# Performance work log

Measured on AMD Instinct MI355X. Metric: run time of the kernel, lower is better.

## Reference

```python
import jax, jax.numpy as jnp
import numpy as np


def setup_inputs() -> dict:
    key = jax.random.key(0)
    k1, k2, k3, k4 = jax.random.split(key, 4)
    B, T, C, H = 8, 2048, 768, 64
    x = jax.random.normal(k1, (B, T, C), dtype=jnp.float32)
    # nn.Linear(n_embd, head_size, bias=False): weight [H, C]; stored here as [C, H] for x @ W
    Wk = jax.random.normal(k2, (C, H), dtype=jnp.float32) * (C ** -0.5)
    Wq = jax.random.normal(k3, (C, H), dtype=jnp.float32) * (C ** -0.5)
    Wv = jax.random.normal(k4, (C, H), dtype=jnp.float32) * (C ** -0.5)
    return {"x": x, "Wk": Wk, "Wq": Wq, "Wv": Wv}


def reference(x, Wk, Wq, Wv):
    # x: [B, T, C]
    C = x.shape[-1]
    k = jnp.einsum("btc,ch->bth", x, Wk)  # [B, T, H]
    q = jnp.einsum("btc,ch->bth", x, Wq)  # [B, T, H]
    v = jnp.einsum("btc,ch->bth", x, Wv)  # [B, T, H]
    # NOTE: source scales by C**-0.5 where C = n_embd (input channels), not head_size
    wei = jnp.einsum("bth,bsh->bts", q, k) * (C ** -0.5)  # [B, T, T]
    wei = jax.nn.softmax(wei, axis=-1)
    # dropout p=0.0 (eval): identity
    out = jnp.einsum("bts,bsh->bth", wei, v)  # [B, T, H]
    return out
```

## Files before the change

kernel.cpp:

```cpp
#include <hip/hip_runtime.h>


typedef __attribute__((ext_vector_type(4))) float f32x4;
typedef __attribute__((ext_vector_type(8))) unsigned short u16x8;
typedef __attribute__((ext_vector_type(8))) __bf16 bf16x8;
typedef __attribute__((ext_vector_type(8))) _Float16 f16x8;

#define LDR 72
#define LDT 40
#define KSCALE (0.03608439182435161f * 1.4426950408889634f)
#define PBIAS 4.0f

__device__ __forceinline__ unsigned short f2bf(float f) {
  unsigned int u = __float_as_uint(f);
  u += 0x7FFFu + ((u >> 16) & 1u);
  return (unsigned short)(u >> 16);
}
__device__ __forceinline__ unsigned short hi16(float f) {
  return (unsigned short)(__float_as_uint(f) >> 16);
}
__device__ __forceinline__ f32x4 mfma_bf16(u16x8 a, u16x8 b, f32x4 c) {
  return __builtin_amdgcn_mfma_f32_16x16x32_bf16(
      __builtin_bit_cast(bf16x8, a), __builtin_bit_cast(bf16x8, b), c, 0, 0, 0);
}
__device__ __forceinline__ void cp32B(unsigned short* dst, const unsigned short* src) {
  *(u16x8*)dst = *(const u16x8*)src;
  *(u16x8*)(dst + 8) = *(const u16x8*)(src + 8);
}

__global__ __launch_bounds__(256) void wconv_k(const float* __restrict__ Wk,
                                               const float* __restrict__ Wq,
                                               const float* __restrict__ Wv,
                                               unsigned short* __restrict__ wt) {
  __shared__ unsigned short tr[64 * LDR];
  const int w = blockIdx.x / 12;
  const int kt = blockIdx.x - w * 12;
  const float* W = (w == 0) ? Wk : ((w == 1) ? Wq : Wv);
  const int tid = threadIdx.x;
  const int kr = tid >> 2;
  const int n0 = (tid & 3) * 16;
  const f32x4* src = (const f32x4*)(W + (size_t)(kt * 64 + kr) * 64 + n0);
  f32x4 a0 = src[0], a1 = src[1], a2 = src[2], a3 = src[3];
#pragma unroll
  for (int j = 0; j < 4; ++j) {
    tr[(n0 + j) * LDR + kr] = f2bf(a0[j]);
    tr[(n0 + 4 + j) * LDR + kr] = f2bf(a1[j]);
    tr[(n0 + 8 + j) * LDR + kr] = f2bf(a2[j]);
    tr[(n0 + 12 + j) * LDR + kr] = f2bf(a3[j]);
  }
  __syncthreads();
  const int n = tid >> 2, kc = (tid & 3) * 16;
  cp32B(&wt[(size_t)(w * 64 + n) * 768 + kt * 64 + kc], &tr[n * LDR + kc]);
}

__global__ __launch_bounds__(256) void proj_k(const float* __restrict__ x,
                                              const unsigned short* __restrict__ wt,
                                              unsigned short* __restrict__ kg,
                                              unsigned short* __restrict__ qg,
                                              unsigned short* __restrict__ vt) {
  __shared__ unsigned short x_s[32 * LDR];
  __shared__ unsigned short w_s[192 * LDR];
  __shared__ unsigned short vt_s[64 * LDT];
  const int tid = threadIdx.x;
  const int wv = tid >> 6, lane = tid & 63, c = lane & 15, quad = lane >> 4;
  const int m0 = blockIdx.x * 32;
  const int rowg = wv & 1;
  const int nfb = (wv >> 1) * 6;
  const int srow = tid >> 3;
  const int sc8 = (tid & 7) * 8;

  f32x4 acc[6];
#pragma unroll
  for (int i = 0; i < 6; ++i) acc[i] = f32x4{0.f, 0.f, 0.f, 0.f};

  f32x4 xf0, xf1;
  u16x8 wf[6];
  {
    const f32x4* s = (const f32x4*)(x + (size_t)(m0 + srow) * 768 + sc8);
    xf0 = s[0]; xf1 = s[1];
  }
#pragma unroll
  for (int i = 0; i < 6; ++i)
    wf[i] = *(const u16x8*)&wt[(size_t)(srow + 32 * i) * 768 + sc8];

  for (int kc = 0; kc < 768; kc += 64) {
    {
      u16x8 u;
#pragma unroll
      for (int j = 0; j < 4; ++j) { u[j] = f2bf(xf0[j]); u[4 + j] = f2bf(xf1[j]); }
      *(u16x8*)&x_s[srow * LDR + sc8] = u;
    }
#pragma unroll
    for (int i = 0; i < 6; ++i)
      *(u16x8*)&w_s[(srow + 32 * i) * LDR + sc8] = wf[i];
    __syncthreads();
    if (kc + 64 < 768) {
      const f32x4* s = (const f32x4*)(x + (size_t)(m0 + srow) * 768 + kc + 64 + sc8);
      xf0 = s[0]; xf1 = s[1];
#pragma unroll
      for (int i = 0; i < 6; ++i)
        wf[i] = *(const u16x8*)&wt[(size_t)(srow + 32 * i) * 768 + kc + 64 + sc8];
    }
#pragma unroll
    for (int k32 = 0; k32 < 2; ++k32) {
      u16x8 a = *(const u16x8*)&x_s[(rowg * 16 + c) * LDR + k32 * 32 + quad * 8];
#pragma unroll
      for (int j = 0; j < 6; ++j) {
        u16x8 b = *(const u16x8*)&w_s[((nfb + j) * 16 + c) * LDR + k32 * 32 + quad * 8];
        acc[j] = mfma_bf16(a, b, acc[j]);
      }
    }
    __syncthreads();
  }
  const int r0 = rowg * 16 + quad * 4;
#pragma unroll
  for (int j = 0; j < 6; ++j) {
    const int nf = nfb + j;
    if (nf < 4) {
#pragma unroll
      for (int r = 0; r < 4; ++r)
        kg[(size_t)(m0 + r0 + r) * 64 + nf * 16 + c] = f2bf(acc[j][r]);
    } else if (nf < 8) {
#pragma unroll
      for (int r = 0; r < 4; ++r)
        qg[(size_t)(m0 + r0 + r) * 64 + (nf - 4) * 16 + c] = f2bf(acc[j][r] * KSCALE);
    } else {
#pragma unroll
      for (int r = 0; r < 4; ++r)
        vt_s[((nf - 8) * 16 + c) * LDT + r0 + r] = f2bf(acc[j][r]);
    }
  }
  __syncthreads();
  {
    const int h = tid >> 2, c8 = (tid & 3) * 8;
    const int b = m0 >> 11, tb = m0 & 2047;
    *(u16x8*)(vt + (size_t)b * 131072 + (size_t)h * 2048 + tb + c8) =
        *(const u16x8*)&vt_s[h * LDT + c8];
  }
}

__global__ __launch_bounds__(256, 4) void attn_k(const unsigned short* __restrict__ qg,
                                                 const unsigned short* __restrict__ kg,
                                                 const unsigned short* __restrict__ vt,
                                                 _Float16* __restrict__ part,
                                                 float* __restrict__ lsum) {
  __shared__ unsigned short k_s[64 * LDR];
  __shared__ unsigned short v_s[64 * LDR];
  __shared__ unsigned short p_s[64 * LDR];
  const int tid = threadIdx.x;
  const int wv = tid >> 6, lane = tid & 63, c = lane & 15, quad = lane >> 4;
  const int bq = blockIdx.x;
  const int qt = blockIdx.y;
  const int sc = blockIdx.z;
  const int tq0 = qt * 64;
  const int srow = tid >> 2, sch = (tid & 3) * 16;
  const int s_beg = sc << 9, s_end = s_beg + 512;

  const unsigned short* kbase = kg + (size_t)bq * 131072;
  const unsigned short* vbase = vt + (size_t)bq * 131072;

  u16x8 aq[2];
#pragma unroll
  for (int k32 = 0; k32 < 2; ++k32)
    aq[k32] = *(const u16x8*)(qg + (size_t)(bq * 2048 + tq0 + wv * 16 + c) * 64 +
                              k32 * 32 + quad * 8);

  u16x8 kb0 = *(const u16x8*)(kbase + (size_t)(s_beg + srow) * 64 + sch);
  u16x8 kb1 = *(const u16x8*)(kbase + (size_t)(s_beg + srow) * 64 + sch + 8);
  u16x8 vb0 = *(const u16x8*)(vbase + (size_t)srow * 2048 + s_beg + sch);
  u16x8 vb1 = *(const u16x8*)(vbase + (size_t)srow * 2048 + s_beg + sch + 8);

  u16x8 ones;
#pragma unroll
  for (int j = 0; j < 8; ++j) ones[j] = 0x3F80;

  f32x4 o_acc[4], l_acc;
#pragma unroll
  for (int hf = 0; hf < 4; ++hf) o_acc[hf] = f32x4{0.f, 0.f, 0.f, 0.f};
  l_acc = f32x4{0.f, 0.f, 0.f, 0.f};

  for (int s0 = s_beg; s0 < s_end; s0 += 64) {
    *(u16x8*)&k_s[srow * LDR + sch] = kb0;
    *(u16x8*)&k_s[srow * LDR + sch + 8] = kb1;
    *(u16x8*)&v_s[srow * LDR + sch] = vb0;
    *(u16x8*)&v_s[srow * LDR + sch + 8] = vb1;
    __syncthreads();
    if (s0 + 64 < s_end) {
      kb0 = *(const u16x8*)(kbase + (size_t)(s0 + 64 + srow) * 64 + sch);
      kb1 = *(const u16x8*)(kbase + (size_t)(s0 + 64 + srow) * 64 + sch + 8);
      vb0 = *(const u16x8*)(vbase + (size_t)srow * 2048 + s0 + 64 + sch);
      vb1 = *(const u16x8*)(vbase + (size_t)srow * 2048 + s0 + 64 + sch + 8);
    }
    f32x4 sacc[4];
#pragma unroll
    for (int nf = 0; nf < 4; ++nf) sacc[nf] = f32x4{0.f, 0.f, 0.f, 0.f};
#pragma unroll
    for (int k32 = 0; k32 < 2; ++k32) {
#pragma unroll
      for (int nf = 0; nf < 4; ++nf) {
        u16x8 b = *(const u16x8*)&k_s[(nf * 16 + c) * LDR + k32 * 32 + quad * 8];
        sacc[nf] = mfma_bf16(aq[k32], b, sacc[nf]);
      }
    }
    const int prow = wv * 16 + quad * 4;
#pragma unroll
    for (int nf = 0; nf < 4; ++nf)
#pragma unroll
      for (int r = 0; r < 4; ++r)
        p_s[(prow + r) * LDR + ((nf ^ quad) * 16) + c] =
            hi16(__builtin_amdgcn_exp2f(sacc[nf][r] - PBIAS));
    asm volatile("s_waitcnt lgkmcnt(0)" ::: "memory");
#pragma unroll
    for (int k32 = 0; k32 < 2; ++k32) {
      const int chunkP = (2 * k32 + (quad >> 1)) ^ (c >> 2);
      u16x8 ap = *(const u16x8*)&p_s[(wv * 16 + c) * LDR + chunkP * 16 + (quad & 1) * 8];
#pragma unroll
      for (int hf = 0; hf < 4; ++hf) {
        u16x8 bv = *(const u16x8*)&v_s[(hf * 16 + c) * LDR + k32 * 32 + quad * 8];
        o_acc[hf] = mfma_bf16(ap, bv, o_acc[hf]);
      }
      l_acc = mfma_bf16(ap, ones, l_acc);
    }
    __syncthreads();
  }
  const int pbase = (bq * 32 + qt) * 4 + sc;
  _Float16* po = part + (size_t)pbase * 4096;
#pragma unroll
  for (int hf = 0; hf < 4; ++hf)
#pragma unroll
    for (int r = 0; r < 4; ++r)
      po[(wv * 16 + quad * 4 + r) * 64 + hf * 16 + c] = (_Float16)o_acc[hf][r];
  if (c == 0) {
#pragma unroll
    for (int r = 0; r < 4; ++r)
      lsum[pbase * 64 + wv * 16 + quad * 4 + r] = l_acc[r];
  }
}

__global__ __launch_bounds__(256) void comb_k(const _Float16* __restrict__ part,
                                              const float* __restrict__ lsum,
                                              float* __restrict__ out) {
  const int bq = blockIdx.x, qh = blockIdx.y;
  const int qt = qh >> 1;
  const int row = (qh & 1) * 32 + (threadIdx.x >> 3);
  const int h0 = (threadIdx.x & 7) * 8;
  const int base = (bq * 32 + qt) * 4;
  float acc[8];
#pragma unroll
  for (int j = 0; j < 8; ++j) acc[j] = 0.f;
  float l = 0.f;
#pragma unroll
  for (int c4 = 0; c4 < 4; ++c4) {
    l += lsum[(base + c4) * 64 + row];
    f16x8 p = *(const f16x8*)(part + (size_t)(base + c4) * 4096 + row * 64 + h0);
#pragma unroll
    for (int j = 0; j < 8; ++j) acc[j] += (float)p[j];
  }
  const float inv = 1.0f / l;
  float* op = out + (size_t)(bq * 2048 + qt * 64 + row) * 64 + h0;
#pragma unroll
  for (int j = 0; j < 8; ++j) op[j] = acc[j] * inv;
}

extern "C" void kernel_launch(void* const* d_in, const int* in_sizes, int n_in,
                              void* d_out, int out_size, void* d_ws, size_t ws_size,
                              hipStream_t stream) {
  const float* x = (const float*)d_in[0];
  const float* Wk = (const float*)d_in[1];
  const float* Wq = (const float*)d_in[2];
  const float* Wv = (const float*)d_in[3];
  char* ws = (char*)d_ws;
  unsigned short* kg = (unsigned short*)(ws);
  unsigned short* qg = (unsigned short*)(ws + (size_t)(2 << 20));
  unsigned short* vt = (unsigned short*)(ws + (size_t)(4 << 20));
  unsigned short* wt = (unsigned short*)(ws + (size_t)(6 << 20));
  _Float16* part = (_Float16*)(ws + (size_t)(7 << 20));
  float* lsum = (float*)(ws + (size_t)(15 << 20));
  float* out = (float*)d_out;

  hipLaunchKernelGGL(wconv_k, dim3(36), dim3(256), 0, stream, Wk, Wq, Wv, wt);
  hipLaunchKernelGGL(proj_k, dim3(512), dim3(256), 0, stream, x, wt, kg, qg, vt);
  hipLaunchKernelGGL(attn_k, dim3(8, 32, 4), dim3(256), 0, stream, qg, kg, vt, part, lsum);
  hipLaunchKernelGGL(comb_k, dim3(8, 64), dim3(256), 0, stream, part, lsum, out);
}
```

Before: 122.1 us.

## Fuse all four stages into one cooperative kernel with grid syncs

Merges weight conversion, projection, attention and combine into a single persistent cooperative kernel of 1024 blocks, with grid-wide barriers between the stages. The aim is to remove three kernel launch gaps and their tail effects. In exchange, every stage now shares one shared-memory allocation, sized for the largest stage, and a 4-blocks-per-CU occupancy bound. Each grid.sync also adds a global barrier, and small stages leave most blocks idle. If the device does not support cooperative launch or cannot fit 4 blocks per CU, the original four separate launches are used instead.

Measured after the change: 121.8 us. About the same (-0.2%).

```diff
diff --git a/kernel.cpp b/kernel.cpp
--- a/kernel.cpp
+++ b/kernel.cpp
@@ -1,4 +1,5 @@
 #include <hip/hip_runtime.h>
+#include <hip/hip_cooperative_groups.h>
 
 
 typedef __attribute__((ext_vector_type(4))) float f32x4;
@@ -10,6 +11,7 @@
 #define LDT 40
 #define KSCALE (0.03608439182435161f * 1.4426950408889634f)
 #define PBIAS 4.0f
+#define SMEM_USHORTS 18688
 
 __device__ __forceinline__ unsigned short f2bf(float f) {
   unsigned int u = __float_as_uint(f);
@@ -28,15 +30,14 @@
   *(u16x8*)(dst + 8) = *(const u16x8*)(src + 8);
 }
 
-__global__ __launch_bounds__(256) void wconv_k(const float* __restrict__ Wk,
-                                               const float* __restrict__ Wq,
-                                               const float* __restrict__ Wv,
-                                               unsigned short* __restrict__ wt) {
-  __shared__ unsigned short tr[64 * LDR];
-  const int w = blockIdx.x / 12;
-  const int kt = blockIdx.x - w * 12;
+__device__ __forceinline__ void wconv_body(int bid, int tid, unsigned short* tr,
+                                           const float* __restrict__ Wk,
+                                           const float* __restrict__ Wq,
+                                           const float* __restrict__ Wv,
+                                           unsigned short* __restrict__ wt) {
+  const int w = bid / 12;
+  const int kt = bid - w * 12;
   const float* W = (w == 0) ? Wk : ((w == 1) ? Wq : Wv);
-  const int tid = threadIdx.x;
   const int kr = tid >> 2;
   const int n0 = (tid & 3) * 16;
   const f32x4* src = (const f32x4*)(W + (size_t)(kt * 64 + kr) * 64 + n0);
@@ -53,17 +54,17 @@
   cp32B(&wt[(size_t)(w * 64 + n) * 768 + kt * 64 + kc], &tr[n * LDR + kc]);
 }
 
-__global__ __launch_bounds__(256) void proj_k(const float* __restrict__ x,
-                                              const unsigned short* __restrict__ wt,
-                                              unsigned short* __restrict__ kg,
-                                              unsigned short* __restrict__ qg,
-                                              unsigned short* __restrict__ vt) {
-  __shared__ unsigned short x_s[32 * LDR];
-  __shared__ unsigned short w_s[192 * LDR];
-  __shared__ unsigned short vt_s[64 * LDT];
-  const int tid = threadIdx.x;
+__device__ __forceinline__ void proj_body(int bid, int tid, unsigned short* smem,
+                                          const float* __restrict__ x,
+                                          const unsigned short* __restrict__ wt,
+                                          unsigned short* __restrict__ kg,
+                                          unsigned short* __restrict__ qg,
+                                          unsigned short* __restrict__ vt) {
+  unsigned short* x_s = smem;
+  unsigned short* w_s = smem + 32 * LDR;
+  unsigned short* vt_s = smem + 224 * LDR;
   const int wv = tid >> 6, lane = tid & 63, c = lane & 15, quad = lane >> 4;
-  const int m0 = blockIdx.x * 32;
+  const int m0 = bid * 32;
   const int rowg = wv & 1;
   const int nfb = (wv >> 1) * 6;
   const int srow = tid >> 3;
@@ -139,19 +140,17 @@
   }
 }
 
-__global__ __launch_bounds__(256, 4) void attn_k(const unsigned short* __restrict__ qg,
-                                                 const unsigned short* __restrict__ kg,
-                                                 const unsigned short* __restrict__ vt,
-                                                 _Float16* __restrict__ part,
-                                                 float* __restrict__ lsum) {
-  __shared__ unsigned short k_s[64 * LDR];
-  __shared__ unsigned short v_s[64 * LDR];
-  __shared__ unsigned short p_s[64 * LDR];
-  const int tid = threadIdx.x;
+__device__ __forceinline__ void attn_body(int bq, int qt, int sc, int tid,
+                                          unsigned short* smem,
+                                          const unsigned short* __restrict__ qg,
+                                          const unsigned short* __restrict__ kg,
+                                          const unsigned short* __restrict__ vt,
+                                          _Float16* __restrict__ part,
+                                          float* __restrict__ lsum) {
+  unsigned short* k_s = smem;
+  unsigned short* v_s = smem + 64 * LDR;
+  unsigned short* p_s = smem + 128 * LDR;
   const int wv = tid >> 6, lane = tid & 63, c = lane & 15, quad = lane >> 4;
-  const int bq = blockIdx.x;
-  const int qt = blockIdx.y;
-  const int sc = blockIdx.z;
   const int tq0 = qt * 64;
   const int srow = tid >> 2, sch = (tid & 3) * 16;
   const int s_beg = sc << 9, s_end = s_beg + 512;
@@ -237,29 +236,79 @@
   }
 }
 
+__device__ __forceinline__ void comb_body(int bq, int qh, int tid,
+                                          const _Float16* __restrict__ part,
+                                          const float* __restrict__ lsum,
+                                          float* __restrict__ out) {
+  const int qt = qh >> 1;
+  const int row = (qh & 1) * 32 + (tid >> 3);
+  const int h0 = (tid & 7) * 8;
+  const int base = (bq * 32 + qt) * 4;
+  float acc[8];
+#pragma unroll
+  for (int j = 0; j < 8; ++j) acc[j] = 0.f;
+  float l = 0.f;
+#pragma unroll
+  for (int c4 = 0; c4 < 4; ++c4) {
+    l += lsum[(base + c4) * 64 + row];
+    f16x8 p = *(const f16x8*)(part + (size_t)(base + c4) * 4096 + row * 64 + h0);
+#pragma unroll
+    for (int j = 0; j < 8; ++j) acc[j] += (float)p[j];
+  }
+  const float inv = 1.0f / l;
+  float* op = out + (size_t)(bq * 2048 + qt * 64 + row) * 64 + h0;
+#pragma unroll
+  for (int j = 0; j < 8; ++j) op[j] = acc[j] * inv;
+}
+
+__global__ __launch_bounds__(256, 4) void fused_k(
+    const float* __restrict__ x, const float* __restrict__ Wk,
+    const float* __restrict__ Wq, const float* __restrict__ Wv,
+    unsigned short* __restrict__ wt, unsigned short* __restrict__ kg,
+    unsigned short* __restrict__ qg, unsigned short* __restrict__ vt,
+    _Float16* __restrict__ part, float* __restrict__ lsum,
+    float* __restrict__ out) {
+  __shared__ unsigned short smem[SMEM_USHORTS];
+  const int tid = threadIdx.x;
+  const int bid = blockIdx.x;
+  cooperative_groups::grid_group grid = cooperative_groups::this_grid();
+
+  if (bid < 36) wconv_body(bid, tid, smem, Wk, Wq, Wv, wt);
+  grid.sync();
+  if (bid < 512) proj_body(bid, tid, smem, x, wt, kg, qg, vt);
+  grid.sync();
+  attn_body(bid & 7, (bid >> 3) & 31, bid >> 8, tid, smem, qg, kg, vt, part, lsum);
+  grid.sync();
+  if (bid < 512) comb_body(bid & 7, bid >> 3, tid, part, lsum, out);
+}
+
+__global__ __launch_bounds__(256) void wconv_k(const float* __restrict__ Wk,
+                                               const float* __restrict__ Wq,
+                                               const float* __restrict__ Wv,
+                                               unsigned short* __restrict__ wt) {
+  __shared__ unsigned short tr[64 * LDR];
+  wconv_body(blockIdx.x, threadIdx.x, tr, Wk, Wq, Wv, wt);
+}
+__global__ __launch_bounds__(256) void proj_k(const float* __restrict__ x,
+                                              const unsigned short* __restrict__ wt,
+                                              unsigned short* __restrict__ kg,
+                                              unsigned short* __restrict__ qg,
+                                              unsigned short* __restrict__ vt) {
+  __shared__ unsigned short smem[SMEM_USHORTS];
+  proj_body(blockIdx.x, threadIdx.x, smem, x, wt, kg, qg, vt);
+}
+__global__ __launch_bounds__(256, 4) void attn_k(const unsigned short* __restrict__ qg,
+                                                 const unsigned short* __restrict__ kg,
+                                                 const unsigned short* __restrict__ vt,
+                                                 _Float16* __restrict__ part,
+                                                 float* __restrict__ lsum) {
+  __shared__ unsigned short smem[192 * LDR];
+  attn_body(blockIdx.x, blockIdx.y, blockIdx.z, threadIdx.x, smem, qg, kg, vt, part, lsum);
+}
 __global__ __launch_bounds__(256) void comb_k(const _Float16* __restrict__ part,
                                               const float* __restrict__ lsum,
                                               float* __restrict__ out) {
-  const int bq = blockIdx.x, qh = blockIdx.y;
-  const int qt = qh >> 1;
-  const int row = (qh & 1) * 32 + (threadIdx.x >> 3);
-  const int h0 = (threadIdx.x & 7) * 8;
-  const int base = (bq * 32 + qt) * 4;
-  float acc[8];
-#pragma unroll
-  for (int j = 0; j < 8; ++j) acc[j] = 0.f;
-  float l = 0.f;
-#pragma unroll
-  for (int c4 = 0; c4 < 4; ++c4) {
-    l += lsum[(base + c4) * 64 + row];
-    f16x8 p = *(const f16x8*)(part + (size_t)(base + c4) * 4096 + row * 64 + h0);
-#pragma unroll
-    for (int j = 0; j < 8; ++j) acc[j] += (float)p[j];
-  }
-  const float inv = 1.0f / l;
-  float* op = out + (size_t)(bq * 2048 + qt * 64 + row) * 64 + h0;
-#pragma unroll
-  for (int j = 0; j < 8; ++j) op[j] = acc[j] * inv;
+  comb_body(blockIdx.x, blockIdx.y, threadIdx.x, part, lsum, out);
 }
 
 extern "C" void kernel_launch(void* const* d_in, const int* in_sizes, int n_in,
@@ -278,8 +327,25 @@
   float* lsum = (float*)(ws + (size_t)(15 << 20));
   float* out = (float*)d_out;
 
-  hipLaunchKernelGGL(wconv_k, dim3(36), dim3(256), 0, stream, Wk, Wq, Wv, wt);
-  hipLaunchKernelGGL(proj_k, dim3(512), dim3(256), 0, stream, x, wt, kg, qg, vt);
-  hipLaunchKernelGGL(attn_k, dim3(8, 32, 4), dim3(256), 0, stream, qg, kg, vt, part, lsum);
-  hipLaunchKernelGGL(comb_k, dim3(8, 64), dim3(256), 0, stream, part, lsum, out);
-}
+  static int coop = -1;
+  if (coop < 0) {
+    int nb = 0, dev = 0, supp = 0;
+    if (hipOccupancyMaxActiveBlocksPerMultiprocessor(&nb, fused_k, 256, 0) != hipSuccess)
+      nb = 0;
+    hipGetDevice(&dev);
+    hipDeviceGetAttribute(&supp, hipDeviceAttributeCooperativeLaunch, dev);
+    coop = (nb >= 4 && supp != 0) ? 1 : 0;
+  }
+
+  if (coop) {
+    void* args[] = {(void*)&x,  (void*)&Wk,   (void*)&Wq,   (void*)&Wv,
+                    (void*)&wt, (void*)&kg,   (void*)&qg,   (void*)&vt,
+                    (void*)&part, (void*)&lsum, (void*)&out};
+    hipLaunchCooperativeKernel(fused_k, dim3(1024), dim3(256), args, 0, stream);
+  } else {
+    hipLaunchKernelGGL(wconv_k, dim3(36), dim3(256), 0, stream, Wk, Wq, Wv, wt);
+    hipLaunchKernelGGL(proj_k, dim3(512), dim3(256), 0, stream, x, wt, kg, qg, vt);
+    hipLaunchKernelGGL(attn_k, dim3(8, 32, 4), dim3(256), 0, stream, qg, kg, vt, part, lsum);
+    hipLaunchKernelGGL(comb_k, dim3(8, 64), dim3(256), 0, stream, part, lsum, out);
+  }
+}
```

## Load K and V MFMA fragments directly from global memory, dropping LDS staging

Applied to the files above, without the earlier changes.

The attention kernel stops staging K and V tiles through shared memory with block-wide barriers. Each wave now loads its own K and V MFMA operand fragments straight from global memory into registers every iteration, and the __syncthreads calls go away. This removes LDS write/read traffic and barrier stalls, but each of the four waves loads the full K/V tile redundantly. It also loses the register prefetch of the next tile, so global load latency is exposed unless the compiler overlaps it, and register pressure rises.

New measurement: 161.4 us. 32.2% more time.

```diff
diff --git a/kernel.cpp b/kernel.cpp
--- a/kernel.cpp
+++ b/kernel.cpp
@@ -144,8 +144,6 @@
                                                  const unsigned short* __restrict__ vt,
                                                  _Float16* __restrict__ part,
                                                  float* __restrict__ lsum) {
-  __shared__ unsigned short k_s[64 * LDR];
-  __shared__ unsigned short v_s[64 * LDR];
   __shared__ unsigned short p_s[64 * LDR];
   const int tid = threadIdx.x;
   const int wv = tid >> 6, lane = tid & 63, c = lane & 15, quad = lane >> 4;
@@ -153,8 +151,7 @@
   const int qt = blockIdx.y;
   const int sc = blockIdx.z;
   const int tq0 = qt * 64;
-  const int srow = tid >> 2, sch = (tid & 3) * 16;
-  const int s_beg = sc << 9, s_end = s_beg + 512;
+  const int s_beg = sc << 9;
 
   const unsigned short* kbase = kg + (size_t)bq * 131072;
   const unsigned short* vbase = vt + (size_t)bq * 131072;
@@ -165,10 +162,8 @@
     aq[k32] = *(const u16x8*)(qg + (size_t)(bq * 2048 + tq0 + wv * 16 + c) * 64 +
                               k32 * 32 + quad * 8);
 
-  u16x8 kb0 = *(const u16x8*)(kbase + (size_t)(s_beg + srow) * 64 + sch);
-  u16x8 kb1 = *(const u16x8*)(kbase + (size_t)(s_beg + srow) * 64 + sch + 8);
-  u16x8 vb0 = *(const u16x8*)(vbase + (size_t)srow * 2048 + s_beg + sch);
-  u16x8 vb1 = *(const u16x8*)(vbase + (size_t)srow * 2048 + s_beg + sch + 8);
+  const unsigned short* kp = kbase + (size_t)(s_beg + c) * 64 + quad * 8;
+  const unsigned short* vp = vbase + (size_t)c * 2048 + s_beg + quad * 8;
 
   u16x8 ones;
 #pragma unroll
@@ -179,29 +174,28 @@
   for (int hf = 0; hf < 4; ++hf) o_acc[hf] = f32x4{0.f, 0.f, 0.f, 0.f};
   l_acc = f32x4{0.f, 0.f, 0.f, 0.f};
 
-  for (int s0 = s_beg; s0 < s_end; s0 += 64) {
-    *(u16x8*)&k_s[srow * LDR + sch] = kb0;
-    *(u16x8*)&k_s[srow * LDR + sch + 8] = kb1;
-    *(u16x8*)&v_s[srow * LDR + sch] = vb0;
-    *(u16x8*)&v_s[srow * LDR + sch + 8] = vb1;
-    __syncthreads();
-    if (s0 + 64 < s_end) {
-      kb0 = *(const u16x8*)(kbase + (size_t)(s0 + 64 + srow) * 64 + sch);
-      kb1 = *(const u16x8*)(kbase + (size_t)(s0 + 64 + srow) * 64 + sch + 8);
-      vb0 = *(const u16x8*)(vbase + (size_t)srow * 2048 + s0 + 64 + sch);
-      vb1 = *(const u16x8*)(vbase + (size_t)srow * 2048 + s0 + 64 + sch + 8);
-    }
+  for (int t = 0; t < 8; ++t) {
+    u16x8 kf[4][2], vf[4][2];
+#pragma unroll
+    for (int nf = 0; nf < 4; ++nf)
+#pragma unroll
+      for (int k32 = 0; k32 < 2; ++k32)
+        kf[nf][k32] = *(const u16x8*)(kp + nf * 16 * 64 + k32 * 32);
+#pragma unroll
+    for (int hf = 0; hf < 4; ++hf)
+#pragma unroll
+      for (int k32 = 0; k32 < 2; ++k32)
+        vf[hf][k32] = *(const u16x8*)(vp + (size_t)hf * 16 * 2048 + k32 * 32);
+
     f32x4 sacc[4];
 #pragma unroll
     for (int nf = 0; nf < 4; ++nf) sacc[nf] = f32x4{0.f, 0.f, 0.f, 0.f};
 #pragma unroll
-    for (int k32 = 0; k32 < 2; ++k32) {
-#pragma unroll
-      for (int nf = 0; nf < 4; ++nf) {
-        u16x8 b = *(const u16x8*)&k_s[(nf * 16 + c) * LDR + k32 * 32 + quad * 8];
-        sacc[nf] = mfma_bf16(aq[k32], b, sacc[nf]);
-      }
-    }
+    for (int k32 = 0; k32 < 2; ++k32)
+#pragma unroll
+      for (int nf = 0; nf < 4; ++nf)
+        sacc[nf] = mfma_bf16(aq[k32], kf[nf][k32], sacc[nf]);
+
     const int prow = wv * 16 + quad * 4;
 #pragma unroll
     for (int nf = 0; nf < 4; ++nf)
@@ -215,13 +209,12 @@
       const int chunkP = (2 * k32 + (quad >> 1)) ^ (c >> 2);
       u16x8 ap = *(const u16x8*)&p_s[(wv * 16 + c) * LDR + chunkP * 16 + (quad & 1) * 8];
 #pragma unroll
-      for (int hf = 0; hf < 4; ++hf) {
-        u16x8 bv = *(const u16x8*)&v_s[(hf * 16 + c) * LDR + k32 * 32 + quad * 8];
-        o_acc[hf] = mfma_bf16(ap, bv, o_acc[hf]);
-      }
+      for (int hf = 0; hf < 4; ++hf)
+        o_acc[hf] = mfma_bf16(ap, vf[hf][k32], o_acc[hf]);
       l_acc = mfma_bf16(ap, ones, l_acc);
     }
-    __syncthreads();
+    kp += 64 * 64;
+    vp += 64;
   }
   const int pbase = (bq * 32 + qt) * 4 + sc;
   _Float16* po = part + (size_t)pbase * 4096;
```

## Stream projection weights via direct global-to-LDS loads with swizzled double buffer

Applied to the files above, without the earlier changes.

Changes the converted weight layout to k-tile-major with an XOR swizzle, so each 64-wide k slice is contiguous. The projection kernel then loads weights straight into a double-buffered LDS array with global_load_lds, instead of staging them through registers, and reads them back with the swizzled offsets. This is meant to cut register pressure and VGPR-to-LDS store traffic and to reduce bank conflicts. It adds about 48KB of LDS per block, which may lower occupancy, and relies on vmcnt waits for correctness.

After: 122.3 us. Within noise of the previous version (+0.2%).

```diff
diff --git a/kernel.cpp b/kernel.cpp
--- a/kernel.cpp
+++ b/kernel.cpp
@@ -11,6 +11,9 @@
 #define KSCALE (0.03608439182435161f * 1.4426950408889634f)
 #define PBIAS 4.0f
 
+typedef const __attribute__((address_space(1))) unsigned int* gas_u32p;
+typedef __attribute__((address_space(3))) unsigned int* las_u32p;
+
 __device__ __forceinline__ unsigned short f2bf(float f) {
   unsigned int u = __float_as_uint(f);
   u += 0x7FFFu + ((u >> 16) & 1u);
@@ -22,10 +25,6 @@
 __device__ __forceinline__ f32x4 mfma_bf16(u16x8 a, u16x8 b, f32x4 c) {
   return __builtin_amdgcn_mfma_f32_16x16x32_bf16(
       __builtin_bit_cast(bf16x8, a), __builtin_bit_cast(bf16x8, b), c, 0, 0, 0);
-}
-__device__ __forceinline__ void cp32B(unsigned short* dst, const unsigned short* src) {
-  *(u16x8*)dst = *(const u16x8*)src;
-  *(u16x8*)(dst + 8) = *(const u16x8*)(src + 8);
 }
 
 __global__ __launch_bounds__(256) void wconv_k(const float* __restrict__ Wk,
@@ -50,7 +49,14 @@
   }
   __syncthreads();
   const int n = tid >> 2, kc = (tid & 3) * 16;
-  cp32B(&wt[(size_t)(w * 64 + n) * 768 + kt * 64 + kc], &tr[n * LDR + kc]);
+  const int row = w * 64 + n;
+  const int sw = (row & 7) << 4;
+  unsigned short* tbase = wt + (size_t)kt * 12288 + row * 64;
+#pragma unroll
+  for (int jj = 0; jj < 2; ++jj) {
+    const int j16 = kc * 2 + jj * 16;
+    *(u16x8*)&tbase[(j16 ^ sw) >> 1] = *(const u16x8*)&tr[n * LDR + kc + jj * 8];
+  }
 }
 
 __global__ __launch_bounds__(256) void proj_k(const float* __restrict__ x,
@@ -58,8 +64,8 @@
                                               unsigned short* __restrict__ kg,
                                               unsigned short* __restrict__ qg,
                                               unsigned short* __restrict__ vt) {
-  __shared__ unsigned short x_s[32 * LDR];
-  __shared__ unsigned short w_s[192 * LDR];
+  __shared__ __align__(16) unsigned short x_s[32 * LDR];
+  __shared__ __align__(16) unsigned short w_s[2][12288];
   __shared__ unsigned short vt_s[64 * LDT];
   const int tid = threadIdx.x;
   const int wv = tid >> 6, lane = tid & 63, c = lane & 15, quad = lane >> 4;
@@ -68,45 +74,51 @@
   const int nfb = (wv >> 1) * 6;
   const int srow = tid >> 3;
   const int sc8 = (tid & 7) * 8;
+  const int wsw = (c & 7) << 4;
 
   f32x4 acc[6];
 #pragma unroll
   for (int i = 0; i < 6; ++i) acc[i] = f32x4{0.f, 0.f, 0.f, 0.f};
 
+#pragma unroll
+  for (int i = 0; i < 6; ++i)
+    __builtin_amdgcn_global_load_lds(
+        (gas_u32p)(const void*)(wt + i * 2048 + tid * 8),
+        (las_u32p)(void*)(&w_s[0][i * 2048 + tid * 8]), 16, 0, 0);
   f32x4 xf0, xf1;
-  u16x8 wf[6];
   {
     const f32x4* s = (const f32x4*)(x + (size_t)(m0 + srow) * 768 + sc8);
     xf0 = s[0]; xf1 = s[1];
   }
-#pragma unroll
-  for (int i = 0; i < 6; ++i)
-    wf[i] = *(const u16x8*)&wt[(size_t)(srow + 32 * i) * 768 + sc8];
-
-  for (int kc = 0; kc < 768; kc += 64) {
+
+  for (int t = 0; t < 12; ++t) {
     {
       u16x8 u;
 #pragma unroll
       for (int j = 0; j < 4; ++j) { u[j] = f2bf(xf0[j]); u[4 + j] = f2bf(xf1[j]); }
       *(u16x8*)&x_s[srow * LDR + sc8] = u;
     }
-#pragma unroll
-    for (int i = 0; i < 6; ++i)
-      *(u16x8*)&w_s[(srow + 32 * i) * LDR + sc8] = wf[i];
-    __syncthreads();
-    if (kc + 64 < 768) {
-      const f32x4* s = (const f32x4*)(x + (size_t)(m0 + srow) * 768 + kc + 64 + sc8);
+    asm volatile("s_waitcnt vmcnt(0)" ::: "memory");
+    __syncthreads();
+    if (t + 1 < 12) {
+      const f32x4* s = (const f32x4*)(x + (size_t)(m0 + srow) * 768 + (t + 1) * 64 + sc8);
       xf0 = s[0]; xf1 = s[1];
+      const unsigned short* wsrc = wt + (size_t)(t + 1) * 12288;
+      unsigned short* wdst = w_s[(t + 1) & 1];
 #pragma unroll
       for (int i = 0; i < 6; ++i)
-        wf[i] = *(const u16x8*)&wt[(size_t)(srow + 32 * i) * 768 + kc + 64 + sc8];
-    }
+        __builtin_amdgcn_global_load_lds(
+            (gas_u32p)(const void*)(wsrc + i * 2048 + tid * 8),
+            (las_u32p)(void*)(wdst + i * 2048 + tid * 8), 16, 0, 0);
+    }
+    const char* wp = (const char*)w_s[t & 1];
 #pragma unroll
     for (int k32 = 0; k32 < 2; ++k32) {
       u16x8 a = *(const u16x8*)&x_s[(rowg * 16 + c) * LDR + k32 * 32 + quad * 8];
+      const int koff = (k32 * 64 + quad * 16) ^ wsw;
 #pragma unroll
       for (int j = 0; j < 6; ++j) {
-        u16x8 b = *(const u16x8*)&w_s[((nfb + j) * 16 + c) * LDR + k32 * 32 + quad * 8];
+        u16x8 b = *(const u16x8*)(wp + ((nfb + j) * 16 + c) * 128 + koff);
         acc[j] = mfma_bf16(a, b, acc[j]);
       }
     }
```
